# Kernel optimization log

Measured on AMD Instinct MI355X. Metric: run time of the kernel, lower is better.

## Reference

```python
import jax, jax.numpy as jnp
import numpy as np

LN_EPS = 1e-5
SEL_EPS = 1e-12
RANK = 16


def _layernorm2d(t, w, b):
    # t: [S, r, M]; normalize jointly over last two dims (torch LayerNorm([r, M]))
    mu = jnp.mean(t, axis=(1, 2), keepdims=True)
    var = jnp.mean(jnp.square(t - mu), axis=(1, 2), keepdims=True)
    return (t - mu) * jax.lax.rsqrt(var + LN_EPS) * w + b


def _tensor_product_construct(wl, dim, lnw1, lnb1, lnw2, lnb2):
    # wl: [4, S, r, L] -> [S, r, dim]
    S, r, L = wl.shape[1], wl.shape[2], wl.shape[3]
    w01 = (wl[0][..., :, None] * wl[1][..., None, :]).reshape(S, r, L * L)
    w01 = _layernorm2d(w01, lnw1, lnb1)
    w23 = (wl[2][..., :, None] * wl[3][..., None, :]).reshape(S, r, L * L)
    w23 = _layernorm2d(w23, lnw2, lnb2)
    w0123 = (w01[..., :, None] * w23[..., None, :]).reshape(S, r, -1)
    return w0123[:, :, :dim]


def setup_inputs() -> dict:
    key = jax.random.key(0)
    ks = jax.random.split(key, 8)
    bs, seq, d = 8, 2048, 4096
    n_tasks, n_skills, rank, leaf = 64, 8, RANK, 8
    x = jax.random.normal(ks[0], (bs, seq, d), dtype=jnp.float32)
    task_ids = jax.random.randint(ks[1], (bs,), 0, n_tasks)
    weight = jax.random.normal(ks[2], (d, d), dtype=jnp.float32) * 0.02
    bias = jax.random.normal(ks[3], (d,), dtype=jnp.float32) * 0.02
    module_logits = jax.random.uniform(ks[4], (n_tasks, n_skills), dtype=jnp.float32, minval=-0.001, maxval=0.001)
    std = (2.0 / (1.0 + 5.0)) ** 0.5 / (d ** 0.5)  # leaky_relu gain / sqrt(in_features)
    wla = jax.random.uniform(ks[5], (4, n_skills, rank, leaf), dtype=jnp.float32, minval=-std, maxval=std)
    wlb = jax.random.uniform(ks[6], (4, n_skills, rank, leaf), dtype=jnp.float32, minval=-std, maxval=std)
    ln1_w = jnp.ones((rank, leaf * leaf), dtype=jnp.float32)
    ln1_b = jnp.zeros((rank, leaf * leaf), dtype=jnp.float32)
    ln2_w = jnp.ones((rank, leaf * leaf), dtype=jnp.float32)
    ln2_b = jnp.zeros((rank, leaf * leaf), dtype=jnp.float32)
    return {"x": x, "task_ids": task_ids, "weight": weight, "bias": bias,
            "module_logits": module_logits, "wla": wla, "wlb": wlb,
            "ln1_w": ln1_w, "ln1_b": ln1_b, "ln2_w": ln2_w, "ln2_b": ln2_b}


def reference(x, task_ids, weight, bias, module_logits, wla, wlb, ln1_w, ln1_b, ln2_w, ln2_b):
    in_f = x.shape[-1]
    out_f = weight.shape[0]
    # --- Polytropon selector (sigmoid + sum-normalize), n_splits = 1 ---
    logits = module_logits[task_ids]                      # [bs, n_skills]
    probs = jax.nn.sigmoid(logits)
    mw = probs / (jnp.sum(probs, axis=-1, keepdims=True) + SEL_EPS)  # [bs, S]
    # --- build LoRA factors via order-4 tensor product ---
    la = _tensor_product_construct(wla, in_f, ln1_w, ln1_b, ln2_w, ln2_b)   # [S, r, in]
    lb = _tensor_product_construct(wlb, out_f, ln1_w, ln1_b, ln2_w, ln2_b)  # [S, r, out]
    # --- per-example skill mixture ---
    A = jnp.einsum('bs,srd->bdr', mw, la)  # [bs, in, r]
    B = jnp.einsum('bs,srd->brd', mw, lb)  # [bs, r, out]
    h = jnp.einsum('bti,bir->btr', x, A)
    adapter_out = jnp.einsum('btr,bro->bto', h, B) / RANK
    return x @ weight.T + bias + adapter_out
```

## Files before the change

### kernel.cpp

```cpp
#include <hip/hip_runtime.h>
#include <hip/hip_bf16.h>
#include <stdint.h>

#define LN_EPS 1e-5f

typedef __bf16 bf16x8 __attribute__((ext_vector_type(8)));
typedef float f32x4 __attribute__((ext_vector_type(4)));

__device__ __forceinline__ unsigned short f2bf(float x) {
  unsigned u = __float_as_uint(x);
  return (unsigned short)((u + 0x7fffu + ((u >> 16) & 1u)) >> 16);
}

__device__ __forceinline__ void gll16(const void* g, void* l) {
  __builtin_amdgcn_global_load_lds((__attribute__((address_space(1))) void*)g,
                                   (__attribute__((address_space(3))) void*)l, 16, 0, 0);
}

__global__ __launch_bounds__(256) void k_construct(
    const float* __restrict__ wla, const float* __restrict__ wlb,
    const float* __restrict__ ln1w, const float* __restrict__ ln1b,
    const float* __restrict__ ln2w, const float* __restrict__ ln2b,
    float* __restrict__ la, float* __restrict__ lb) {
  const int s = blockIdx.x;
  const int t = threadIdx.x;
  __shared__ float w01[1024];
  __shared__ float w23[1024];
  __shared__ float red[8];
  for (int g = 0; g < 2; ++g) {
    const float* wl = g ? wlb : wla;
    for (int half = 0; half < 2; ++half) {
      const float* lnw  = half ? ln2w : ln1w;
      const float* lnbv = half ? ln2b : ln1b;
      const float* w0 = wl + (2*half + 0)*1024 + s*128;
      const float* w1 = wl + (2*half + 1)*1024 + s*128;
      float* buf = half ? w23 : w01;
      float v[4];
      float sum = 0.f, sumsq = 0.f;
      #pragma unroll
      for (int q = 0; q < 4; ++q) {
        int idx = t + 256*q;
        int r = idx >> 6, m = idx & 63;
        float val = w0[r*8 + (m >> 3)] * w1[r*8 + (m & 7)];
        v[q] = val; sum += val; sumsq += val*val;
      }
      #pragma unroll
      for (int off = 32; off; off >>= 1) {
        sum   += __shfl_down(sum, off);
        sumsq += __shfl_down(sumsq, off);
      }
      if ((t & 63) == 0) { red[t >> 6] = sum; red[4 + (t >> 6)] = sumsq; }
      __syncthreads();
      float fs  = red[0] + red[1] + red[2] + red[3];
      float fss = red[4] + red[5] + red[6] + red[7];
      float mu  = fs * (1.f/1024.f);
      float var = fss * (1.f/1024.f) - mu*mu;
      float rs  = rsqrtf(var + LN_EPS);
      __syncthreads();
      #pragma unroll
      for (int q = 0; q < 4; ++q) {
        int idx = t + 256*q;
        buf[idx] = (v[q] - mu) * rs * lnw[idx] + lnbv[idx];
      }
      __syncthreads();
    }
    float* dst = (g ? lb : la) + s*65536;
    for (int q = 0; q < 256; ++q) {
      int f = t + 256*q;
      int rb = (f >> 12) << 6;
      dst[f] = w01[rb + ((f >> 6) & 63)] * w23[rb + (f & 63)];
    }
    __syncthreads();
  }
}

__global__ __launch_bounds__(256) void k_mix(
    const float* __restrict__ la, const float* __restrict__ lb,
    const float* __restrict__ module_logits, const int* __restrict__ task_ids,
    float* __restrict__ A, unsigned short* __restrict__ Bmb) {
  int gid = blockIdx.x*256 + threadIdx.x;
  int b = gid >> 12, d = gid & 4095;
  int task = task_ids[b];
  float mwv[8]; float ssum = 0.f;
  #pragma unroll
  for (int s = 0; s < 8; ++s) {
    float p = 1.f / (1.f + expf(-module_logits[task*8 + s]));
    mwv[s] = p; ssum += p;
  }
  float inv = 1.f / (ssum + 1e-12f);
  unsigned pk[8];
  #pragma unroll
  for (int r = 0; r < 16; ++r) {
    float av = 0.f, bv = 0.f;
    #pragma unroll
    for (int s = 0; s < 8; ++s) {
      float w = mwv[s] * inv;
      av += w * la[(s*16 + r)*4096 + d];
      bv += w * lb[(s*16 + r)*4096 + d];
    }
    A[(b*16 + r)*4096 + d] = av;
    unsigned hv = f2bf(bv);
    if (r & 1) pk[r >> 1] |= hv << 16; else pk[r >> 1] = hv;
  }
  uint4* dst = (uint4*)(Bmb + (size_t)gid*32);
  uint4 a0; a0.x = pk[0]; a0.y = pk[1]; a0.z = pk[2]; a0.w = pk[3];
  uint4 a1; a1.x = pk[4]; a1.y = pk[5]; a1.z = pk[6]; a1.w = pk[7];
  uint4 z;  z.x = 0; z.y = 0; z.z = 0; z.w = 0;
  dst[0] = a0; dst[1] = a1; dst[2] = z; dst[3] = z;
}

__global__ __launch_bounds__(256) void k_castw(const float* __restrict__ w,
                                               unsigned short* __restrict__ wb) {
  int i = blockIdx.x*256 + threadIdx.x;
  float4 v = ((const float4*)w)[i];
  uint2 o;
  o.x = (unsigned)f2bf(v.x) | ((unsigned)f2bf(v.y) << 16);
  o.y = (unsigned)f2bf(v.z) | ((unsigned)f2bf(v.w) << 16);
  ((uint2*)wb)[i] = o;
}

__global__ __launch_bounds__(256) void k_rowh(
    const float* __restrict__ x, const float* __restrict__ A,
    unsigned short* __restrict__ xb, unsigned short* __restrict__ hb) {
  int row = blockIdx.x;
  int b = row >> 11;
  int t = threadIdx.x;
  const float* xrow = x + (size_t)row*4096;
  const float* Ab = A + b*65536;
  float p[16];
  #pragma unroll
  for (int r = 0; r < 16; ++r) p[r] = 0.f;
  #pragma unroll
  for (int c = 0; c < 4; ++c) {
    int d0 = c*1024 + t*4;
    float4 xv = *(const float4*)(xrow + d0);
    ushort4 o;
    o.x = f2bf(xv.x); o.y = f2bf(xv.y); o.z = f2bf(xv.z); o.w = f2bf(xv.w);
    *(ushort4*)(xb + (size_t)row*4096 + d0) = o;
    #pragma unroll
    for (int r = 0; r < 16; ++r) {
      float4 av = *(const float4*)(Ab + r*4096 + d0);
      p[r] += xv.x*av.x + xv.y*av.y + xv.z*av.z + xv.w*av.w;
    }
  }
  #pragma unroll
  for (int r = 0; r < 16; ++r)
    #pragma unroll
    for (int off = 32; off; off >>= 1) p[r] += __shfl_down(p[r], off);
  __shared__ float red[4][16];
  int wid = t >> 6, lane = t & 63;
  if (lane == 0) {
    #pragma unroll
    for (int r = 0; r < 16; ++r) red[wid][r] = p[r];
  }
  __syncthreads();
  if (t < 16) {
    float h = red[0][t] + red[1][t] + red[2][t] + red[3][t];
    hb[(size_t)row*32 + t] = f2bf(h * (1.0f/16.0f));
  } else if (t < 32) {
    hb[(size_t)row*32 + t] = 0;
  }
}

__global__ __launch_bounds__(256) void k_gemm(
    const unsigned short* __restrict__ xb, const unsigned short* __restrict__ wb,
    const unsigned short* __restrict__ hb, const unsigned short* __restrict__ Bmb,
    const float* __restrict__ bias, float* __restrict__ out) {
  __shared__ int4 smem_[1024];
  char* lds = (char*)smem_;
  const int tid = threadIdx.x;
  const int nt = blockIdx.x & 31, mt = blockIdx.x >> 5;
  const int row0 = mt << 7, col0 = nt << 7;
  const int b = row0 >> 11;
  const int wid = tid >> 6, lane = tid & 63;
  const int wr = wid >> 1, wc = wid & 1;

  size_t srcA[2], srcB[2], srcAh[2], srcBh[2];
  #pragma unroll
  for (int k = 0; k < 2; ++k) {
    int r = k*64 + (tid >> 2);
    int cc = (tid & 3) ^ ((r >> 1) & 3);
    srcA[k]  = (size_t)(row0 + r)*4096 + cc*8;
    srcB[k]  = (size_t)(col0 + r)*4096 + cc*8;
    srcAh[k] = (size_t)(row0 + r)*32 + cc*8;
    srcBh[k] = ((size_t)b*4096 + col0 + r)*32 + cc*8;
  }
  char* ldsA[2] = { lds + wid*1024,        lds + 4096  + wid*1024 };
  char* ldsB[2] = { lds + 8192 + wid*1024, lds + 12288 + wid*1024 };

  int aoff[4], boff[4];
  #pragma unroll
  for (int mf = 0; mf < 4; ++mf) {
    int r = wr*64 + mf*16 + (lane & 15);
    aoff[mf] = r*64 + (((lane >> 4) ^ ((r >> 1) & 3)) << 4);
  }
  #pragma unroll
  for (int nf = 0; nf < 4; ++nf) {
    int r = wc*64 + nf*16 + (lane & 15);
    boff[nf] = 8192 + r*64 + (((lane >> 4) ^ ((r >> 1) & 3)) << 4);
  }

  f32x4 zero = {0.f, 0.f, 0.f, 0.f};
  f32x4 acc[4][4];
  #pragma unroll
  for (int i = 0; i < 4; ++i)
    #pragma unroll
    for (int j = 0; j < 4; ++j) acc[i][j] = zero;

  for (int it = 0; it < 128; ++it) {
    const size_t ko = (size_t)it*32;
    gll16(xb + srcA[0] + ko, ldsA[0]);
    gll16(xb + srcA[1] + ko, ldsA[1]);
    gll16(wb + srcB[0] + ko, ldsB[0]);
    gll16(wb + srcB[1] + ko, ldsB[1]);
    __syncthreads();
    bf16x8 af[4], bfr[4];
    #pragma unroll
    for (int mf = 0; mf < 4; ++mf) af[mf] = *(const bf16x8*)(lds + aoff[mf]);
    #pragma unroll
    for (int nf = 0; nf < 4; ++nf) bfr[nf] = *(const bf16x8*)(lds + boff[nf]);
    #pragma unroll
    for (int mf = 0; mf < 4; ++mf)
      #pragma unroll
      for (int nf = 0; nf < 4; ++nf)
        acc[mf][nf] = __builtin_amdgcn_mfma_f32_16x16x32_bf16(af[mf], bfr[nf], acc[mf][nf], 0, 0, 0);
    __syncthreads();
  }
  gll16(hb + srcAh[0], ldsA[0]);
  gll16(hb + srcAh[1], ldsA[1]);
  gll16(Bmb + srcBh[0], ldsB[0]);
  gll16(Bmb + srcBh[1], ldsB[1]);
  __syncthreads();
  {
    bf16x8 af[4], bfr[4];
    #pragma unroll
    for (int mf = 0; mf < 4; ++mf) af[mf] = *(const bf16x8*)(lds + aoff[mf]);
    #pragma unroll
    for (int nf = 0; nf < 4; ++nf) bfr[nf] = *(const bf16x8*)(lds + boff[nf]);
    #pragma unroll
    for (int mf = 0; mf < 4; ++mf)
      #pragma unroll
      for (int nf = 0; nf < 4; ++nf)
        acc[mf][nf] = __builtin_amdgcn_mfma_f32_16x16x32_bf16(af[mf], bfr[nf], acc[mf][nf], 0, 0, 0);
  }
  float bv[4];
  #pragma unroll
  for (int nf = 0; nf < 4; ++nf) bv[nf] = bias[col0 + wc*64 + nf*16 + (lane & 15)];
  #pragma unroll
  for (int mf = 0; mf < 4; ++mf) {
    int rowb = row0 + wr*64 + mf*16 + ((lane >> 4) << 2);
    #pragma unroll
    for (int nf = 0; nf < 4; ++nf) {
      int col = col0 + wc*64 + nf*16 + (lane & 15);
      #pragma unroll
      for (int q = 0; q < 4; ++q)
        out[(size_t)(rowb + q)*4096 + col] = acc[mf][nf][q] + bv[nf];
    }
  }
}

extern "C" void kernel_launch(void* const* d_in, const int* in_sizes, int n_in,
                              void* d_out, int out_size, void* d_ws, size_t ws_size,
                              hipStream_t stream) {
  const float* x             = (const float*)d_in[0];
  const int*   task_ids      = (const int*)d_in[1];
  const float* weight        = (const float*)d_in[2];
  const float* bias          = (const float*)d_in[3];
  const float* module_logits = (const float*)d_in[4];
  const float* wla           = (const float*)d_in[5];
  const float* wlb           = (const float*)d_in[6];
  const float* ln1w          = (const float*)d_in[7];
  const float* ln1b          = (const float*)d_in[8];
  const float* ln2w          = (const float*)d_in[9];
  const float* ln2b          = (const float*)d_in[10];
  float* out = (float*)d_out;

  char* ws = (char*)d_ws;
  unsigned short* xb = (unsigned short*)(ws);
  unsigned short* wb = (unsigned short*)(ws + 134217728);
  float* la = (float*)(ws + 134217728 + 33554432);
  float* lb = la + 524288;
  float* A  = lb + 524288;
  unsigned short* Bmb = (unsigned short*)(A + 524288);
  unsigned short* hb  = Bmb + 1048576;

  k_construct<<<8, 256, 0, stream>>>(wla, wlb, ln1w, ln1b, ln2w, ln2b, la, lb);
  k_mix<<<128, 256, 0, stream>>>(la, lb, module_logits, task_ids, A, Bmb);
  k_castw<<<16384, 256, 0, stream>>>(weight, wb);
  k_rowh<<<16384, 256, 0, stream>>>(x, A, xb, hb);
  k_gemm<<<4096, 256, 0, stream>>>(xb, wb, hb, Bmb, bias, out);
}
```

Measured before the change: 1.478 ms.

## Replace GEMM with 256x256 tile, double-buffered LDS pipeline and setprio scheduling

Replaces the 128x128 single-buffered bf16 MFMA GEMM with a 256x256 tile, 512-thread kernel. It uses a 128-byte K-step, double-buffered LDS and staged global_load_lds issues interleaved with MFMA phases. It adds explicit vmcnt/lgkmcnt waits, sched barriers, s_setprio and an XCD-aware block swizzle. The LoRA pad width goes from 32 to 64 columns so the adapter rank step fits the new K-step, and k_rowh is reorganised to handle 32 rows per block with 8-lane reductions. The aim is to hide global load latency and raise MFMA utilisation, at the cost of large LDS use (128 KB) and more complex synchronisation.

```diff
diff --git a/kernel.cpp b/kernel.cpp
--- a/kernel.cpp
+++ b/kernel.cpp
@@ -102,11 +102,12 @@
     unsigned hv = f2bf(bv);
     if (r & 1) pk[r >> 1] |= hv << 16; else pk[r >> 1] = hv;
   }
-  uint4* dst = (uint4*)(Bmb + (size_t)gid*32);
+  uint4* dst = (uint4*)(Bmb + (size_t)gid*64);
   uint4 a0; a0.x = pk[0]; a0.y = pk[1]; a0.z = pk[2]; a0.w = pk[3];
   uint4 a1; a1.x = pk[4]; a1.y = pk[5]; a1.z = pk[6]; a1.w = pk[7];
   uint4 z;  z.x = 0; z.y = 0; z.z = 0; z.w = 0;
-  dst[0] = a0; dst[1] = a1; dst[2] = z; dst[3] = z;
+  dst[0] = a0; dst[1] = a1;
+  dst[2] = z; dst[3] = z; dst[4] = z; dst[5] = z; dst[6] = z; dst[7] = z;
 }
 
 __global__ __launch_bounds__(256) void k_castw(const float* __restrict__ w,
@@ -122,139 +123,209 @@
 __global__ __launch_bounds__(256) void k_rowh(
     const float* __restrict__ x, const float* __restrict__ A,
     unsigned short* __restrict__ xb, unsigned short* __restrict__ hb) {
-  int row = blockIdx.x;
-  int b = row >> 11;
-  int t = threadIdx.x;
-  const float* xrow = x + (size_t)row*4096;
-  const float* Ab = A + b*65536;
+  const int tid = threadIdx.x;
+  const int rl = tid >> 3, seg = tid & 7;
+  const int row = blockIdx.x * 32 + rl;
+  const int b = (blockIdx.x * 32) >> 11;
+  const float* xrow = x + (size_t)row * 4096;
+  const float* Ab = A + b * 65536;
+  unsigned short* xbrow = xb + (size_t)row * 4096;
   float p[16];
   #pragma unroll
   for (int r = 0; r < 16; ++r) p[r] = 0.f;
-  #pragma unroll
-  for (int c = 0; c < 4; ++c) {
-    int d0 = c*1024 + t*4;
+  for (int i = 0; i < 128; ++i) {
+    int d0 = (i * 8 + seg) * 4;
     float4 xv = *(const float4*)(xrow + d0);
-    ushort4 o;
-    o.x = f2bf(xv.x); o.y = f2bf(xv.y); o.z = f2bf(xv.z); o.w = f2bf(xv.w);
-    *(ushort4*)(xb + (size_t)row*4096 + d0) = o;
+    ushort4 o; o.x = f2bf(xv.x); o.y = f2bf(xv.y); o.z = f2bf(xv.z); o.w = f2bf(xv.w);
+    *(ushort4*)(xbrow + d0) = o;
     #pragma unroll
     for (int r = 0; r < 16; ++r) {
-      float4 av = *(const float4*)(Ab + r*4096 + d0);
-      p[r] += xv.x*av.x + xv.y*av.y + xv.z*av.z + xv.w*av.w;
-    }
-  }
-  #pragma unroll
-  for (int r = 0; r < 16; ++r)
-    #pragma unroll
-    for (int off = 32; off; off >>= 1) p[r] += __shfl_down(p[r], off);
-  __shared__ float red[4][16];
-  int wid = t >> 6, lane = t & 63;
-  if (lane == 0) {
-    #pragma unroll
-    for (int r = 0; r < 16; ++r) red[wid][r] = p[r];
-  }
-  __syncthreads();
-  if (t < 16) {
-    float h = red[0][t] + red[1][t] + red[2][t] + red[3][t];
-    hb[(size_t)row*32 + t] = f2bf(h * (1.0f/16.0f));
-  } else if (t < 32) {
-    hb[(size_t)row*32 + t] = 0;
-  }
-}
-
-__global__ __launch_bounds__(256) void k_gemm(
+      float4 av = *(const float4*)(Ab + r * 4096 + d0);
+      p[r] += xv.x * av.x + xv.y * av.y + xv.z * av.z + xv.w * av.w;
+    }
+  }
+  #pragma unroll
+  for (int r = 0; r < 16; ++r) {
+    p[r] += __shfl_down(p[r], 4, 8);
+    p[r] += __shfl_down(p[r], 2, 8);
+    p[r] += __shfl_down(p[r], 1, 8);
+  }
+  unsigned short* hrow = hb + (size_t)row * 64;
+  if (seg == 0) {
+    unsigned pk[8];
+    #pragma unroll
+    for (int r = 0; r < 16; ++r) {
+      unsigned hv = f2bf(p[r] * 0.0625f);
+      if (r & 1) pk[r >> 1] |= hv << 16; else pk[r >> 1] = hv;
+    }
+    uint4 v0; v0.x = pk[0]; v0.y = pk[1]; v0.z = pk[2]; v0.w = pk[3];
+    uint4 v1; v1.x = pk[4]; v1.y = pk[5]; v1.z = pk[6]; v1.w = pk[7];
+    ((uint4*)hrow)[0] = v0; ((uint4*)hrow)[1] = v1;
+  } else if (seg < 4) {
+    uint4 z; z.x = z.y = z.z = z.w = 0;
+    ((uint4*)hrow)[seg * 2] = z; ((uint4*)hrow)[seg * 2 + 1] = z;
+  }
+}
+
+#define DS_A(BOFF, m, ks) (*(const bf16x8*)(ldsc + (BOFF) + abase[m] + (ks) * 64))
+#define DS_B(BOFF, n, ks) (*(const bf16x8*)(ldsc + (BOFF) + bbase[n] + (ks) * 64))
+
+#define VM6 asm volatile("s_waitcnt vmcnt(6)" ::: "memory");
+#define VM0 asm volatile("s_waitcnt vmcnt(0)" ::: "memory");
+
+#define TILE(BOFF, VMSTMT) { \
+  bf16x8 b0f[4], b1f[4], a0f[4], a1f[4], a2f[4], a3f[4]; \
+   \
+  _Pragma("unroll") for (int n = 0; n < 4; ++n) { b0f[n] = DS_B(BOFF,n,0); b1f[n] = DS_B(BOFF,n,1); } \
+  _Pragma("unroll") for (int m = 0; m < 4; ++m) a0f[m] = DS_A(BOFF,m,0); \
+  issue(); \
+  __builtin_amdgcn_sched_barrier(0); \
+  __builtin_amdgcn_s_barrier(); \
+  asm volatile("s_waitcnt lgkmcnt(0)" ::: "memory"); \
+  __builtin_amdgcn_sched_barrier(0); \
+  __builtin_amdgcn_s_setprio(1); \
+  _Pragma("unroll") for (int m = 0; m < 4; ++m) \
+    _Pragma("unroll") for (int n = 0; n < 4; ++n) \
+      acc[m][n] = __builtin_amdgcn_mfma_f32_16x16x32_bf16(a0f[m], b0f[n], acc[m][n], 0, 0, 0); \
+  __builtin_amdgcn_s_setprio(0); \
+  __builtin_amdgcn_sched_barrier(0); \
+  __builtin_amdgcn_s_barrier(); \
+   \
+  _Pragma("unroll") for (int m = 0; m < 4; ++m) a1f[m] = DS_A(BOFF,m,1); \
+  _Pragma("unroll") for (int m = 0; m < 4; ++m) a2f[m] = DS_A(BOFF,4+m,0); \
+  issue(); \
+  __builtin_amdgcn_sched_barrier(0); \
+  __builtin_amdgcn_s_barrier(); \
+  asm volatile("s_waitcnt lgkmcnt(0)" ::: "memory"); \
+  __builtin_amdgcn_sched_barrier(0); \
+  __builtin_amdgcn_s_setprio(1); \
+  _Pragma("unroll") for (int m = 0; m < 4; ++m) \
+    _Pragma("unroll") for (int n = 0; n < 4; ++n) \
+      acc[m][n] = __builtin_amdgcn_mfma_f32_16x16x32_bf16(a1f[m], b1f[n], acc[m][n], 0, 0, 0); \
+  __builtin_amdgcn_s_setprio(0); \
+  __builtin_amdgcn_sched_barrier(0); \
+  __builtin_amdgcn_s_barrier(); \
+   \
+  _Pragma("unroll") for (int m = 0; m < 4; ++m) a3f[m] = DS_A(BOFF,4+m,1); \
+  issue(); \
+  __builtin_amdgcn_sched_barrier(0); \
+  __builtin_amdgcn_s_barrier(); \
+  asm volatile("s_waitcnt lgkmcnt(0)" ::: "memory"); \
+  __builtin_amdgcn_sched_barrier(0); \
+  __builtin_amdgcn_s_setprio(1); \
+  _Pragma("unroll") for (int m = 0; m < 4; ++m) \
+    _Pragma("unroll") for (int n = 0; n < 4; ++n) \
+      acc[4+m][n] = __builtin_amdgcn_mfma_f32_16x16x32_bf16(a2f[m], b0f[n], acc[4+m][n], 0, 0, 0); \
+  __builtin_amdgcn_s_setprio(0); \
+  __builtin_amdgcn_sched_barrier(0); \
+  __builtin_amdgcn_s_barrier(); \
+   \
+  issue(); \
+  __builtin_amdgcn_sched_barrier(0); \
+  VMSTMT \
+  __builtin_amdgcn_s_barrier(); \
+  __builtin_amdgcn_s_setprio(1); \
+  _Pragma("unroll") for (int m = 0; m < 4; ++m) \
+    _Pragma("unroll") for (int n = 0; n < 4; ++n) \
+      acc[4+m][n] = __builtin_amdgcn_mfma_f32_16x16x32_bf16(a3f[m], b1f[n], acc[4+m][n], 0, 0, 0); \
+  __builtin_amdgcn_s_setprio(0); \
+  __builtin_amdgcn_sched_barrier(0); \
+  __builtin_amdgcn_s_barrier(); \
+}
+
+__global__ __launch_bounds__(512, 2) void k_gemm256(
     const unsigned short* __restrict__ xb, const unsigned short* __restrict__ wb,
     const unsigned short* __restrict__ hb, const unsigned short* __restrict__ Bmb,
     const float* __restrict__ bias, float* __restrict__ out) {
-  __shared__ int4 smem_[1024];
-  char* lds = (char*)smem_;
+  __shared__ int4 smem[8192];
+  char* ldsc = (char*)smem;
   const int tid = threadIdx.x;
-  const int nt = blockIdx.x & 31, mt = blockIdx.x >> 5;
-  const int row0 = mt << 7, col0 = nt << 7;
+  const int bid = blockIdx.x;
+  const int swz = ((bid & 7) << 7) + (bid >> 3);
+  const int mt = swz >> 4, nt = swz & 15;
+  const int row0 = mt << 8, col0 = nt << 8;
   const int b = row0 >> 11;
   const int wid = tid >> 6, lane = tid & 63;
-  const int wr = wid >> 1, wc = wid & 1;
-
-  size_t srcA[2], srcB[2], srcAh[2], srcBh[2];
-  #pragma unroll
-  for (int k = 0; k < 2; ++k) {
-    int r = k*64 + (tid >> 2);
-    int cc = (tid & 3) ^ ((r >> 1) & 3);
-    srcA[k]  = (size_t)(row0 + r)*4096 + cc*8;
-    srcB[k]  = (size_t)(col0 + r)*4096 + cc*8;
-    srcAh[k] = (size_t)(row0 + r)*32 + cc*8;
-    srcBh[k] = ((size_t)b*4096 + col0 + r)*32 + cc*8;
-  }
-  char* ldsA[2] = { lds + wid*1024,        lds + 4096  + wid*1024 };
-  char* ldsB[2] = { lds + 8192 + wid*1024, lds + 12288 + wid*1024 };
-
-  int aoff[4], boff[4];
-  #pragma unroll
-  for (int mf = 0; mf < 4; ++mf) {
-    int r = wr*64 + mf*16 + (lane & 15);
-    aoff[mf] = r*64 + (((lane >> 4) ^ ((r >> 1) & 3)) << 4);
-  }
-  #pragma unroll
-  for (int nf = 0; nf < 4; ++nf) {
-    int r = wc*64 + nf*16 + (lane & 15);
-    boff[nf] = 8192 + r*64 + (((lane >> 4) ^ ((r >> 1) & 3)) << 4);
-  }
-
-  f32x4 zero = {0.f, 0.f, 0.f, 0.f};
-  f32x4 acc[4][4];
-  #pragma unroll
-  for (int i = 0; i < 4; ++i)
-    #pragma unroll
-    for (int j = 0; j < 4; ++j) acc[i][j] = zero;
-
-  for (int it = 0; it < 128; ++it) {
-    const size_t ko = (size_t)it*32;
-    gll16(xb + srcA[0] + ko, ldsA[0]);
-    gll16(xb + srcA[1] + ko, ldsA[1]);
-    gll16(wb + srcB[0] + ko, ldsB[0]);
-    gll16(wb + srcB[1] + ko, ldsB[1]);
-    __syncthreads();
-    bf16x8 af[4], bfr[4];
-    #pragma unroll
-    for (int mf = 0; mf < 4; ++mf) af[mf] = *(const bf16x8*)(lds + aoff[mf]);
-    #pragma unroll
-    for (int nf = 0; nf < 4; ++nf) bfr[nf] = *(const bf16x8*)(lds + boff[nf]);
-    #pragma unroll
-    for (int mf = 0; mf < 4; ++mf)
-      #pragma unroll
-      for (int nf = 0; nf < 4; ++nf)
-        acc[mf][nf] = __builtin_amdgcn_mfma_f32_16x16x32_bf16(af[mf], bfr[nf], acc[mf][nf], 0, 0, 0);
-    __syncthreads();
-  }
-  gll16(hb + srcAh[0], ldsA[0]);
-  gll16(hb + srcAh[1], ldsA[1]);
-  gll16(Bmb + srcBh[0], ldsB[0]);
-  gll16(Bmb + srcBh[1], ldsB[1]);
-  __syncthreads();
-  {
-    bf16x8 af[4], bfr[4];
-    #pragma unroll
-    for (int mf = 0; mf < 4; ++mf) af[mf] = *(const bf16x8*)(lds + aoff[mf]);
-    #pragma unroll
-    for (int nf = 0; nf < 4; ++nf) bfr[nf] = *(const bf16x8*)(lds + boff[nf]);
-    #pragma unroll
-    for (int mf = 0; mf < 4; ++mf)
-      #pragma unroll
-      for (int nf = 0; nf < 4; ++nf)
-        acc[mf][nf] = __builtin_amdgcn_mfma_f32_16x16x32_bf16(af[mf], bfr[nf], acc[mf][nf], 0, 0, 0);
-  }
+  const int wr = wid >> 2, wc = wid & 3;
+  const int u = lane >> 4, lr = lane & 15;
+
+  int abase[8], bbase[4];
+  #pragma unroll
+  for (int m = 0; m < 8; ++m) {
+    int rowin = m * 16 + lr;
+    abase[m] = (2 + wr) * 16384 + rowin * 128 + ((u << 4) ^ ((rowin & 4) << 3));
+  }
+  #pragma unroll
+  for (int n = 0; n < 4; ++n) {
+    int rowin = (wc & 1) * 64 + n * 16 + lr;
+    bbase[n] = (wc >> 1) * 16384 + rowin * 128 + ((u << 4) ^ ((rowin & 4) << 3));
+  }
+
+  int q0 = tid * 16, q1 = 8192 + tid * 16;
+  int qs0 = q0 ^ (((q0 >> 9) & 1) << 5), qs1 = q1 ^ (((q1 >> 9) & 1) << 5);
+  int rowq0 = qs0 >> 7, colb0 = qs0 & 127;
+  int rowq1 = qs1 >> 7, colb1 = qs1 & 127;
+  const char* xc  = (const char*)xb;
+  const char* wcb = (const char*)wb;
+  const char* srcB0 = wcb + (size_t)(col0 + rowq0) * 8192 + colb0;
+  const char* srcB1 = wcb + (size_t)(col0 + rowq1) * 8192 + colb1;
+  const char* srcA0 = xc  + (size_t)(row0 + rowq0) * 8192 + colb0;
+  const char* srcA1 = xc  + (size_t)(row0 + rowq1) * 8192 + colb1;
+  const char* adB0 = (const char*)Bmb + (size_t)b * 524288 + (size_t)(col0 + rowq0) * 128 + colb0;
+  const char* adB1 = (const char*)Bmb + (size_t)b * 524288 + (size_t)(col0 + rowq1) * 128 + colb1;
+  const char* adA0 = (const char*)hb  + (size_t)(row0 + rowq0) * 128 + colb0;
+  const char* adA1 = (const char*)hb  + (size_t)(row0 + rowq1) * 128 + colb1;
+
+  int H = 0;
+  auto issue = [&]() {
+    int h = H++;
+    if (h > 259) return;
+    int tau = h >> 2, part = h & 3;
+    char* d = ldsc + ((tau & 1) << 16) + part * 16384 + tid * 16;
+    if (tau < 64) {
+      size_t ko = (size_t)tau * 128 + ((part & 1) ? 1048576u : 0u);
+      const char* s0 = ((part & 2) ? srcA0 : srcB0) + ko;
+      const char* s1 = ((part & 2) ? srcA1 : srcB1) + ko;
+      gll16(s0, d); gll16(s1, d + 8192);
+    } else {
+      size_t hi = (part & 1) ? 16384u : 0u;
+      const char* s0 = ((part & 2) ? adA0 : adB0) + hi;
+      const char* s1 = ((part & 2) ? adA1 : adB1) + hi;
+      gll16(s0, d); gll16(s1, d + 8192);
+    }
+  };
+
+  f32x4 acc[8][4];
+  #pragma unroll
+  for (int i = 0; i < 8; ++i)
+    #pragma unroll
+    for (int j = 0; j < 4; ++j) acc[i][j] = (f32x4){0.f, 0.f, 0.f, 0.f};
+
+  for (int i = 0; i < 7; ++i) issue();
+  __builtin_amdgcn_sched_barrier(0);
+  VM6
+  __builtin_amdgcn_s_barrier();
+
+  for (int tt = 0; tt < 31; ++tt) {
+    TILE(0, VM6)
+    TILE(65536, VM6)
+  }
+  TILE(0, VM6)
+  TILE(65536, VM0)
+  TILE(0, )
+
   float bv[4];
   #pragma unroll
-  for (int nf = 0; nf < 4; ++nf) bv[nf] = bias[col0 + wc*64 + nf*16 + (lane & 15)];
-  #pragma unroll
-  for (int mf = 0; mf < 4; ++mf) {
-    int rowb = row0 + wr*64 + mf*16 + ((lane >> 4) << 2);
-    #pragma unroll
-    for (int nf = 0; nf < 4; ++nf) {
-      int col = col0 + wc*64 + nf*16 + (lane & 15);
+  for (int n = 0; n < 4; ++n) bv[n] = bias[col0 + wc * 64 + n * 16 + lr];
+  #pragma unroll
+  for (int m = 0; m < 8; ++m) {
+    int rb = row0 + wr * 128 + m * 16 + u * 4;
+    #pragma unroll
+    for (int n = 0; n < 4; ++n) {
+      int cl = col0 + wc * 64 + n * 16 + lr;
       #pragma unroll
       for (int q = 0; q < 4; ++q)
-        out[(size_t)(rowb + q)*4096 + col] = acc[mf][nf][q] + bv[nf];
+        out[(size_t)(rb + q) * 4096 + cl] = acc[m][n][q] + bv[n];
     }
   }
 }
@@ -276,17 +347,17 @@
   float* out = (float*)d_out;
 
   char* ws = (char*)d_ws;
-  unsigned short* xb = (unsigned short*)(ws);
-  unsigned short* wb = (unsigned short*)(ws + 134217728);
-  float* la = (float*)(ws + 134217728 + 33554432);
-  float* lb = la + 524288;
-  float* A  = lb + 524288;
-  unsigned short* Bmb = (unsigned short*)(A + 524288);
-  unsigned short* hb  = Bmb + 1048576;
+  unsigned short* xb  = (unsigned short*)(ws);
+  unsigned short* wb  = (unsigned short*)(ws + 134217728);
+  float* la           = (float*)(ws + 167772160);
+  float* lb           = (float*)(ws + 169869312);
+  float* A            = (float*)(ws + 171966464);
+  unsigned short* Bmb = (unsigned short*)(ws + 174063616);
+  unsigned short* hb  = (unsigned short*)(ws + 178257920);
 
   k_construct<<<8, 256, 0, stream>>>(wla, wlb, ln1w, ln1b, ln2w, ln2b, la, lb);
   k_mix<<<128, 256, 0, stream>>>(la, lb, module_logits, task_ids, A, Bmb);
   k_castw<<<16384, 256, 0, stream>>>(weight, wb);
-  k_rowh<<<16384, 256, 0, stream>>>(x, A, xb, hb);
-  k_gemm<<<4096, 256, 0, stream>>>(xb, wb, hb, Bmb, bias, out);
-}
+  k_rowh<<<512, 256, 0, stream>>>(x, A, xb, hb);
+  k_gemm256<<<1024, 512, 0, stream>>>(xb, wb, hb, Bmb, bias, out);
+}
```

Result: slower. 2.788 ms (+88.7%).
